# Performance work log

Measured on AMD Instinct MI355X. Metric: run time of the kernel, lower is better.

## Reference

```python
import jax, jax.numpy as jnp
import numpy as np

NUM_EMBEDDINGS = 8192
EMBEDDING_DIM = 64
N_VOXELS = 32768


def setup_inputs() -> dict:
    key = jax.random.key(0)
    k1, k2 = jax.random.split(key)
    z = jax.random.normal(k1, (N_VOXELS, EMBEDDING_DIM), dtype=jnp.float32)
    codebook = jax.random.normal(k2, (NUM_EMBEDDINGS, EMBEDDING_DIM), dtype=jnp.float32)
    return {"z": z, "codebook": codebook}


def reference(z, codebook):
    # Squared euclidean distances [N, K]; argmin is identical to argmin of cdist.
    # d2 = ||z||^2 - 2 z E^T + ||E||^2
    z_sq = jnp.sum(z * z, axis=1, keepdims=True)            # [N, 1]
    e_sq = jnp.sum(codebook * codebook, axis=1)              # [K]
    d2 = z_sq - 2.0 * (z @ codebook.T) + e_sq[None, :]       # [N, K]
    encoding_indices = jnp.argmin(d2, axis=1)                # [N] int

    quantized_feats = codebook[encoding_indices]             # [N, D] gather

    sg = jax.lax.stop_gradient
    commitment_loss = jnp.mean((z - sg(quantized_feats)) ** 2)
    vq_loss = jnp.mean((quantized_feats - sg(z)) ** 2)

    # Straight-through estimator
    quantized = z + sg(quantized_feats - z)                  # [N, D]

    return quantized, vq_loss, commitment_loss, encoding_indices
```

## Files before the change

### kernel.cpp

```cpp
#include <hip/hip_runtime.h>
#include <math.h>

#define N_VOX 32768
#define N_EMB 8192
#define DIM 64
#define NCHUNK 8
#define CODES_PER_CHUNK (N_EMB / NCHUNK)
#define TILES_PER_CHUNK (CODES_PER_CHUNK / 32)
#define NTILES (N_EMB / 32)
#define TILE_BYTES 8192
#define CHUNK_BYTES (TILES_PER_CHUNK * TILE_BYTES)

typedef _Float16 half8 __attribute__((ext_vector_type(8)));
typedef float floatx4 __attribute__((ext_vector_type(4)));

#define FP16_MIN_NORMAL 6.1035156e-5f
#define LO_SCALE 2048.0f

__global__ __launch_bounds__(256) void cbprep_kernel(const float* __restrict__ cb,
                                                     char* __restrict__ stream,
                                                     float* __restrict__ c0arr) {
    __shared__ float red[256];
    int tid  = threadIdx.x;
    int l    = tid & 63;
    int o    = tid >> 6;
    int m    = l & 31;
    int tile = blockIdx.x;
    char* tbase = stream + (size_t)tile * TILE_BYTES;
    int code = tile * 32 + m;
    int kg   = l >> 5;

    const float* p = cb + (size_t)code * DIM + o * 16 + kg * 8;
    float ss = 0.f;
    half8 h, lo;
    #pragma unroll
    for (int j = 0; j < 8; ++j) {
        float x = p[j];
        ss = fmaf(x, x, ss);
        _Float16 hi = (_Float16)x;
        float hf = (float)hi;
        if (fabsf(hf) < FP16_MIN_NORMAL) { hi = (_Float16)0.f; hf = 0.f; }
        h[j]  = hi;
        lo[j] = (_Float16)((x - hf) * LO_SCALE);
    }
    *(half8*)(tbase +        o * 1024 + l * 16) = h;
    *(half8*)(tbase + 4096 + o * 1024 + l * 16) = lo;

    red[tid] = ss;
    __syncthreads();
    if (tid < 32) {
        float s = 0.f;
        #pragma unroll
        for (int q = 0; q < 8; ++q) s += red[tid + q * 32];
        c0arr[tile * 32 + tid] = -1024.0f * s;
    }
}

__global__ __launch_bounds__(512) void scan_kernel(const float* __restrict__ z,
                                                   const char* __restrict__ stream,
                                                   const float* __restrict__ c0arr,
                                                   float* __restrict__ cand_val,
                                                   int* __restrict__ cand_idx) {
    __shared__ __align__(16) char lds[4 * TILE_BYTES + CODES_PER_CHUNK * 4];
    float* c0_lds = (float*)(lds + 4 * TILE_BYTES);
    int tid   = threadIdx.x;
    int l     = tid & 63;
    int w     = tid >> 6;
    int chunk = blockIdx.x & (NCHUNK - 1);
    int rg    = blockIdx.x >> 3;
    int lr    = l & 15;
    int lq    = l >> 4;
    int rowBase = rg * 256 + w * 32;

    half8 zh[2][2], zl[2][2], zhs[2][2];
    #pragma unroll
    for (int r = 0; r < 2; ++r) {
        #pragma unroll
        for (int h = 0; h < 2; ++h) {
            const float* p = z + (size_t)(rowBase + r * 16 + lr) * DIM + h * 32 + lq * 8;
            #pragma unroll
            for (int j = 0; j < 8; ++j) {
                float x = p[j];
                _Float16 hi = (_Float16)x;
                float hf = (float)hi;
                if (fabsf(hf) < FP16_MIN_NORMAL) { hi = (_Float16)0.f; hf = 0.f; }
                zh[r][h][j] = hi;
                zl[r][h][j] = (_Float16)((x - hf) * LO_SCALE);
            }
            zhs[r][h] = zh[r][h] * (_Float16)2048.0f;
        }
    }

    const char*  sbase = stream + (size_t)chunk * CHUNK_BYTES;
    const float* c0p   = c0arr + chunk * CODES_PER_CHUNK;

    float best[16];
    int   bt[16];
    #pragma unroll
    for (int i = 0; i < 16; ++i) { best[i] = -3.4e38f; bt[i] = 0; }

#define STAGE(gt, lb)                                                              \
    do {                                                                           \
        const char* _g = (gt) + w * 1024 + l * 16;                                 \
        char*       _d = (lb) + w * 1024 + l * 16;                                 \
        __builtin_amdgcn_global_load_lds(                                          \
            (const __attribute__((address_space(1))) void*)_g,                     \
            (__attribute__((address_space(3))) void*)_d, 16, 0, 0);                \
    } while (0)

    STAGE(sbase,                          lds);
    STAGE(sbase + (size_t)TILE_BYTES,     lds + TILE_BYTES);
    STAGE(sbase + 2 * (size_t)TILE_BYTES, lds + 2 * TILE_BYTES);
    c0_lds[tid]       = c0p[tid];
    c0_lds[tid + 512] = c0p[tid + 512];
    __syncthreads();

    for (int t = 0; t < TILES_PER_CHUNK; ++t) {
        if (t < TILES_PER_CHUNK - 2)
            asm volatile("s_waitcnt vmcnt(2)" ::: "memory");
        else if (t == TILES_PER_CHUNK - 2)
            asm volatile("s_waitcnt vmcnt(1)" ::: "memory");
        else
            asm volatile("s_waitcnt vmcnt(0)" ::: "memory");
        __builtin_amdgcn_s_barrier();
        asm volatile("" ::: "memory");

        if (t + 3 < TILES_PER_CHUNK)
            STAGE(sbase + (size_t)(t + 3) * TILE_BYTES,
                  lds + ((t + 3) & 3) * TILE_BYTES);

        const char* lb = lds + (t & 3) * TILE_BYTES;
        const char* bp = lb + 512 * lq + 16 * lr;
        half8 bh00 = *(const half8*)(bp +    0);
        half8 bh10 = *(const half8*)(bp +  256);
        half8 bh01 = *(const half8*)(bp + 2048);
        half8 bh11 = *(const half8*)(bp + 2304);
        half8 bl00 = *(const half8*)(bp + 4096);
        half8 bl10 = *(const half8*)(bp + 4352);
        half8 bl01 = *(const half8*)(bp + 6144);
        half8 bl11 = *(const half8*)(bp + 6400);
        float c00 = c0_lds[t * 32 + lr];
        float c01 = c0_lds[t * 32 + 16 + lr];

        floatx4 a00 = {c00, c00, c00, c00};
        floatx4 a01 = {c01, c01, c01, c01};
        floatx4 a10 = {c00, c00, c00, c00};
        floatx4 a11 = {c01, c01, c01, c01};

        a00 = __builtin_amdgcn_mfma_f32_16x16x32_f16(zhs[0][0], bh00, a00, 0, 0, 0);
        a01 = __builtin_amdgcn_mfma_f32_16x16x32_f16(zhs[0][0], bh10, a01, 0, 0, 0);
        a10 = __builtin_amdgcn_mfma_f32_16x16x32_f16(zhs[1][0], bh00, a10, 0, 0, 0);
        a11 = __builtin_amdgcn_mfma_f32_16x16x32_f16(zhs[1][0], bh10, a11, 0, 0, 0);
        a00 = __builtin_amdgcn_mfma_f32_16x16x32_f16(zl[0][0],  bh00, a00, 0, 0, 0);
        a01 = __builtin_amdgcn_mfma_f32_16x16x32_f16(zl[0][0],  bh10, a01, 0, 0, 0);
        a10 = __builtin_amdgcn_mfma_f32_16x16x32_f16(zl[1][0],  bh00, a10, 0, 0, 0);
        a11 = __builtin_amdgcn_mfma_f32_16x16x32_f16(zl[1][0],  bh10, a11, 0, 0, 0);
        a00 = __builtin_amdgcn_mfma_f32_16x16x32_f16(zh[0][0],  bl00, a00, 0, 0, 0);
        a01 = __builtin_amdgcn_mfma_f32_16x16x32_f16(zh[0][0],  bl10, a01, 0, 0, 0);
        a10 = __builtin_amdgcn_mfma_f32_16x16x32_f16(zh[1][0],  bl00, a10, 0, 0, 0);
        a11 = __builtin_amdgcn_mfma_f32_16x16x32_f16(zh[1][0],  bl10, a11, 0, 0, 0);
        a00 = __builtin_amdgcn_mfma_f32_16x16x32_f16(zhs[0][1], bh01, a00, 0, 0, 0);
        a01 = __builtin_amdgcn_mfma_f32_16x16x32_f16(zhs[0][1], bh11, a01, 0, 0, 0);
        a10 = __builtin_amdgcn_mfma_f32_16x16x32_f16(zhs[1][1], bh01, a10, 0, 0, 0);
        a11 = __builtin_amdgcn_mfma_f32_16x16x32_f16(zhs[1][1], bh11, a11, 0, 0, 0);
        a00 = __builtin_amdgcn_mfma_f32_16x16x32_f16(zl[0][1],  bh01, a00, 0, 0, 0);
        a01 = __builtin_amdgcn_mfma_f32_16x16x32_f16(zl[0][1],  bh11, a01, 0, 0, 0);
        a10 = __builtin_amdgcn_mfma_f32_16x16x32_f16(zl[1][1],  bh01, a10, 0, 0, 0);
        a11 = __builtin_amdgcn_mfma_f32_16x16x32_f16(zl[1][1],  bh11, a11, 0, 0, 0);
        a00 = __builtin_amdgcn_mfma_f32_16x16x32_f16(zh[0][1],  bl01, a00, 0, 0, 0);
        a01 = __builtin_amdgcn_mfma_f32_16x16x32_f16(zh[0][1],  bl11, a01, 0, 0, 0);
        a10 = __builtin_amdgcn_mfma_f32_16x16x32_f16(zh[1][1],  bl01, a10, 0, 0, 0);
        a11 = __builtin_amdgcn_mfma_f32_16x16x32_f16(zh[1][1],  bl11, a11, 0, 0, 0);

        #pragma unroll
        for (int i = 0; i < 4; ++i) {
            if (a00[i] > best[ 0 + i]) { best[ 0 + i] = a00[i]; bt[ 0 + i] = t; }
            if (a01[i] > best[ 4 + i]) { best[ 4 + i] = a01[i]; bt[ 4 + i] = t; }
            if (a10[i] > best[ 8 + i]) { best[ 8 + i] = a10[i]; bt[ 8 + i] = t; }
            if (a11[i] > best[12 + i]) { best[12 + i] = a11[i]; bt[12 + i] = t; }
        }
    }
#undef STAGE

    #pragma unroll
    for (int r = 0; r < 2; ++r) {
        #pragma unroll
        for (int i = 0; i < 4; ++i) {
            float v0 = best[r * 8 + i];     int id0 = bt[r * 8 + i] * 32 + lr;
            float v1 = best[r * 8 + 4 + i]; int id1 = bt[r * 8 + 4 + i] * 32 + 16 + lr;
            float v = v0; int id = id0;
            if (v1 > v || (v1 == v && id1 < id)) { v = v1; id = id1; }
            #pragma unroll
            for (int off = 1; off < 16; off <<= 1) {
                float ov = __shfl_xor(v, off, 64);
                int   oi = __shfl_xor(id, off, 64);
                if (ov > v || (ov == v && oi < id)) { v = ov; id = oi; }
            }
            if (lr == 0) {
                int row = rowBase + r * 16 + 4 * lq + i;
                cand_val[chunk * N_VOX + row] = v;
                cand_idx[chunk * N_VOX + row] = chunk * CODES_PER_CHUNK + id;
            }
        }
    }
}

__global__ __launch_bounds__(256) void finalize_kernel(const float* __restrict__ z,
                                                       const float* __restrict__ cb,
                                                       const float* __restrict__ cand_val,
                                                       const int* __restrict__ cand_idx,
                                                       float* __restrict__ out,
                                                       float* __restrict__ partials) {
    int g    = blockIdx.x * 256 + threadIdx.x;
    int row  = g >> 3;
    int c    = g & 7;

    float v  = cand_val[c * N_VOX + row];
    int   id = cand_idx[c * N_VOX + row];
    #pragma unroll
    for (int off = 1; off < 8; off <<= 1) {
        float ov = __shfl_xor(v, off, 8);
        int   oi = __shfl_xor(id, off, 8);
        if (ov > v || (ov == v && oi < id)) { v = ov; id = oi; }
    }

    if (c == 0)
        out[(size_t)N_VOX * DIM + 2 + row] = (float)id;

    const float4* zp = (const float4*)(z  + (size_t)row * DIM + c * 8);
    const float4* qp = (const float4*)(cb + (size_t)id  * DIM + c * 8);
    float4*       op = (float4*)(out + (size_t)row * DIM + c * 8);
    float ss = 0.f;
    #pragma unroll
    for (int d = 0; d < 2; ++d) {
        float4 zt = zp[d], qt = qp[d];
        float dx = qt.x - zt.x, dy = qt.y - zt.y;
        float dz = qt.z - zt.z, dw = qt.w - zt.w;
        float4 o;
        o.x = zt.x + dx; o.y = zt.y + dy;
        o.z = zt.z + dz; o.w = zt.w + dw;
        op[d] = o;
        ss += dx*dx + dy*dy + dz*dz + dw*dw;
    }

    __shared__ float red[256];
    red[threadIdx.x] = ss;
    __syncthreads();
    #pragma unroll
    for (int s = 128; s > 0; s >>= 1) {
        if (threadIdx.x < s) red[threadIdx.x] += red[threadIdx.x + s];
        __syncthreads();
    }
    if (threadIdx.x == 0) partials[blockIdx.x] = red[0];
}

__global__ __launch_bounds__(256) void loss_kernel(const float* __restrict__ partials,
                                                   float* __restrict__ out) {
    __shared__ float red[256];
    red[threadIdx.x] = (partials[threadIdx.x]       + partials[threadIdx.x + 256])
                     + (partials[threadIdx.x + 512] + partials[threadIdx.x + 768]);
    __syncthreads();
    #pragma unroll
    for (int st = 128; st > 0; st >>= 1) {
        if (threadIdx.x < st) red[threadIdx.x] += red[threadIdx.x + st];
        __syncthreads();
    }
    if (threadIdx.x == 0) {
        float mean = red[0] / (float)((size_t)N_VOX * DIM);
        out[(size_t)N_VOX * DIM + 0] = mean;
        out[(size_t)N_VOX * DIM + 1] = mean;
    }
}

extern "C" void kernel_launch(void* const* d_in, const int* in_sizes, int n_in,
                              void* d_out, int out_size, void* d_ws, size_t ws_size,
                              hipStream_t stream) {
    const float* z  = (const float*)d_in[0];
    const float* cb = (const float*)d_in[1];
    float* out = (float*)d_out;

    char*  bstream  = (char*)d_ws;
    float* c0arr    = (float*)(bstream + (size_t)NTILES * TILE_BYTES);
    float* cand_val = c0arr + N_EMB;
    int*   cand_idx = (int*)(cand_val + (size_t)NCHUNK * N_VOX);
    float* partials = (float*)(cand_idx + (size_t)NCHUNK * N_VOX);

    cbprep_kernel  <<<dim3(NTILES), dim3(256), 0, stream>>>(cb, bstream, c0arr);
    scan_kernel    <<<dim3((N_VOX / 256) * NCHUNK), dim3(512), 0, stream>>>(z, bstream, c0arr, cand_val, cand_idx);
    finalize_kernel<<<dim3(N_VOX * 8 / 256), dim3(256), 0, stream>>>(z, cb, cand_val, cand_idx, out, partials);
    loss_kernel    <<<1, 256, 0, stream>>>(partials, out);
}
```

Baseline: 157.7 us.

## Double-buffer LDS fragment loads in registers and raise MFMA priority

Loads the codebook fragments for the next tile from LDS into a second register set while the current tile's MFMAs run, with the loop unrolled by two so the buffers alternate. The global-to-LDS wait counts are adjusted so the next tile is resident one step earlier. MFMA sections are wrapped in s_setprio to favour matrix issue across waves. The aim is to hide LDS read latency behind the matrix instructions, at the cost of more registers and possible occupancy loss.

```diff
diff --git a/kernel.cpp b/kernel.cpp
--- a/kernel.cpp
+++ b/kernel.cpp
@@ -99,6 +99,12 @@
     #pragma unroll
     for (int i = 0; i < 16; ++i) { best[i] = -3.4e38f; bt[i] = 0; }
 
+    struct BF {
+        half8 h00, h10, h01, h11, l00, l10, l01, l11;
+        float ca, cb;
+    };
+    BF fA, fB;
+
 #define STAGE(gt, lb)                                                              \
     do {                                                                           \
         const char* _g = (gt) + w * 1024 + l * 16;                                 \
@@ -108,78 +114,95 @@
             (__attribute__((address_space(3))) void*)_d, 16, 0, 0);                \
     } while (0)
 
+#define LOADB(B, lb, tt)                                                           \
+    do {                                                                           \
+        const char* bp_ = (lb) + 512 * lq + 16 * lr;                               \
+        B.h00 = *(const half8*)(bp_ +    0);                                       \
+        B.h10 = *(const half8*)(bp_ +  256);                                       \
+        B.h01 = *(const half8*)(bp_ + 2048);                                       \
+        B.h11 = *(const half8*)(bp_ + 2304);                                       \
+        B.l00 = *(const half8*)(bp_ + 4096);                                       \
+        B.l10 = *(const half8*)(bp_ + 4352);                                       \
+        B.l01 = *(const half8*)(bp_ + 6144);                                       \
+        B.l11 = *(const half8*)(bp_ + 6400);                                       \
+        B.ca  = c0_lds[(tt) * 32 + lr];                                            \
+        B.cb  = c0_lds[(tt) * 32 + 16 + lr];                                       \
+    } while (0)
+
+#define COMPUTE(B, t)                                                              \
+    do {                                                                           \
+        floatx4 a00 = {B.ca, B.ca, B.ca, B.ca};                                    \
+        floatx4 a01 = {B.cb, B.cb, B.cb, B.cb};                                    \
+        floatx4 a10 = {B.ca, B.ca, B.ca, B.ca};                                    \
+        floatx4 a11 = {B.cb, B.cb, B.cb, B.cb};                                    \
+        __builtin_amdgcn_s_setprio(1);                                             \
+        a00 = __builtin_amdgcn_mfma_f32_16x16x32_f16(zhs[0][0], B.h00, a00, 0, 0, 0); \
+        a01 = __builtin_amdgcn_mfma_f32_16x16x32_f16(zhs[0][0], B.h10, a01, 0, 0, 0); \
+        a10 = __builtin_amdgcn_mfma_f32_16x16x32_f16(zhs[1][0], B.h00, a10, 0, 0, 0); \
+        a11 = __builtin_amdgcn_mfma_f32_16x16x32_f16(zhs[1][0], B.h10, a11, 0, 0, 0); \
+        a00 = __builtin_amdgcn_mfma_f32_16x16x32_f16(zl[0][0],  B.h00, a00, 0, 0, 0); \
+        a01 = __builtin_amdgcn_mfma_f32_16x16x32_f16(zl[0][0],  B.h10, a01, 0, 0, 0); \
+        a10 = __builtin_amdgcn_mfma_f32_16x16x32_f16(zl[1][0],  B.h00, a10, 0, 0, 0); \
+        a11 = __builtin_amdgcn_mfma_f32_16x16x32_f16(zl[1][0],  B.h10, a11, 0, 0, 0); \
+        a00 = __builtin_amdgcn_mfma_f32_16x16x32_f16(zh[0][0],  B.l00, a00, 0, 0, 0); \
+        a01 = __builtin_amdgcn_mfma_f32_16x16x32_f16(zh[0][0],  B.l10, a01, 0, 0, 0); \
+        a10 = __builtin_amdgcn_mfma_f32_16x16x32_f16(zh[1][0],  B.l00, a10, 0, 0, 0); \
+        a11 = __builtin_amdgcn_mfma_f32_16x16x32_f16(zh[1][0],  B.l10, a11, 0, 0, 0); \
+        a00 = __builtin_amdgcn_mfma_f32_16x16x32_f16(zhs[0][1], B.h01, a00, 0, 0, 0); \
+        a01 = __builtin_amdgcn_mfma_f32_16x16x32_f16(zhs[0][1], B.h11, a01, 0, 0, 0); \
+        a10 = __builtin_amdgcn_mfma_f32_16x16x32_f16(zhs[1][1], B.h01, a10, 0, 0, 0); \
+        a11 = __builtin_amdgcn_mfma_f32_16x16x32_f16(zhs[1][1], B.h11, a11, 0, 0, 0); \
+        a00 = __builtin_amdgcn_mfma_f32_16x16x32_f16(zl[0][1],  B.h01, a00, 0, 0, 0); \
+        a01 = __builtin_amdgcn_mfma_f32_16x16x32_f16(zl[0][1],  B.h11, a01, 0, 0, 0); \
+        a10 = __builtin_amdgcn_mfma_f32_16x16x32_f16(zl[1][1],  B.h01, a10, 0, 0, 0); \
+        a11 = __builtin_amdgcn_mfma_f32_16x16x32_f16(zl[1][1],  B.h11, a11, 0, 0, 0); \
+        a00 = __builtin_amdgcn_mfma_f32_16x16x32_f16(zh[0][1],  B.l01, a00, 0, 0, 0); \
+        a01 = __builtin_amdgcn_mfma_f32_16x16x32_f16(zh[0][1],  B.l11, a01, 0, 0, 0); \
+        a10 = __builtin_amdgcn_mfma_f32_16x16x32_f16(zh[1][1],  B.l01, a10, 0, 0, 0); \
+        a11 = __builtin_amdgcn_mfma_f32_16x16x32_f16(zh[1][1],  B.l11, a11, 0, 0, 0); \
+        __builtin_amdgcn_s_setprio(0);                                             \
+        _Pragma("unroll")                                                          \
+        for (int i = 0; i < 4; ++i) {                                              \
+            if (a00[i] > best[ 0 + i]) { best[ 0 + i] = a00[i]; bt[ 0 + i] = (t); } \
+            if (a01[i] > best[ 4 + i]) { best[ 4 + i] = a01[i]; bt[ 4 + i] = (t); } \
+            if (a10[i] > best[ 8 + i]) { best[ 8 + i] = a10[i]; bt[ 8 + i] = (t); } \
+            if (a11[i] > best[12 + i]) { best[12 + i] = a11[i]; bt[12 + i] = (t); } \
+        }                                                                          \
+    } while (0)
+
+#define BODY(t, CUR, NXT)                                                          \
+    do {                                                                           \
+        if ((t) < TILES_PER_CHUNK - 2)                                             \
+            asm volatile("s_waitcnt vmcnt(1)" ::: "memory");                       \
+        else                                                                       \
+            asm volatile("s_waitcnt vmcnt(0)" ::: "memory");                       \
+        __builtin_amdgcn_s_barrier();                                              \
+        asm volatile("" ::: "memory");                                             \
+        if ((t) + 3 < TILES_PER_CHUNK)                                             \
+            STAGE(sbase + (size_t)((t) + 3) * TILE_BYTES,                          \
+                  lds + (((t) + 3) & 3) * TILE_BYTES);                             \
+        if ((t) + 1 < TILES_PER_CHUNK)                                             \
+            LOADB(NXT, lds + (((t) + 1) & 3) * TILE_BYTES, (t) + 1);               \
+        COMPUTE(CUR, (t));                                                         \
+    } while (0)
+
     STAGE(sbase,                          lds);
     STAGE(sbase + (size_t)TILE_BYTES,     lds + TILE_BYTES);
     STAGE(sbase + 2 * (size_t)TILE_BYTES, lds + 2 * TILE_BYTES);
     c0_lds[tid]       = c0p[tid];
     c0_lds[tid + 512] = c0p[tid + 512];
+    asm volatile("s_waitcnt vmcnt(2)" ::: "memory");
     __syncthreads();
-
-    for (int t = 0; t < TILES_PER_CHUNK; ++t) {
-        if (t < TILES_PER_CHUNK - 2)
-            asm volatile("s_waitcnt vmcnt(2)" ::: "memory");
-        else if (t == TILES_PER_CHUNK - 2)
-            asm volatile("s_waitcnt vmcnt(1)" ::: "memory");
-        else
-            asm volatile("s_waitcnt vmcnt(0)" ::: "memory");
-        __builtin_amdgcn_s_barrier();
-        asm volatile("" ::: "memory");
-
-        if (t + 3 < TILES_PER_CHUNK)
-            STAGE(sbase + (size_t)(t + 3) * TILE_BYTES,
-                  lds + ((t + 3) & 3) * TILE_BYTES);
-
-        const char* lb = lds + (t & 3) * TILE_BYTES;
-        const char* bp = lb + 512 * lq + 16 * lr;
-        half8 bh00 = *(const half8*)(bp +    0);
-        half8 bh10 = *(const half8*)(bp +  256);
-        half8 bh01 = *(const half8*)(bp + 2048);
-        half8 bh11 = *(const half8*)(bp + 2304);
-        half8 bl00 = *(const half8*)(bp + 4096);
-        half8 bl10 = *(const half8*)(bp + 4352);
-        half8 bl01 = *(const half8*)(bp + 6144);
-        half8 bl11 = *(const half8*)(bp + 6400);
-        float c00 = c0_lds[t * 32 + lr];
-        float c01 = c0_lds[t * 32 + 16 + lr];
-
-        floatx4 a00 = {c00, c00, c00, c00};
-        floatx4 a01 = {c01, c01, c01, c01};
-        floatx4 a10 = {c00, c00, c00, c00};
-        floatx4 a11 = {c01, c01, c01, c01};
-
-        a00 = __builtin_amdgcn_mfma_f32_16x16x32_f16(zhs[0][0], bh00, a00, 0, 0, 0);
-        a01 = __builtin_amdgcn_mfma_f32_16x16x32_f16(zhs[0][0], bh10, a01, 0, 0, 0);
-        a10 = __builtin_amdgcn_mfma_f32_16x16x32_f16(zhs[1][0], bh00, a10, 0, 0, 0);
-        a11 = __builtin_amdgcn_mfma_f32_16x16x32_f16(zhs[1][0], bh10, a11, 0, 0, 0);
-        a00 = __builtin_amdgcn_mfma_f32_16x16x32_f16(zl[0][0],  bh00, a00, 0, 0, 0);
-        a01 = __builtin_amdgcn_mfma_f32_16x16x32_f16(zl[0][0],  bh10, a01, 0, 0, 0);
-        a10 = __builtin_amdgcn_mfma_f32_16x16x32_f16(zl[1][0],  bh00, a10, 0, 0, 0);
-        a11 = __builtin_amdgcn_mfma_f32_16x16x32_f16(zl[1][0],  bh10, a11, 0, 0, 0);
-        a00 = __builtin_amdgcn_mfma_f32_16x16x32_f16(zh[0][0],  bl00, a00, 0, 0, 0);
-        a01 = __builtin_amdgcn_mfma_f32_16x16x32_f16(zh[0][0],  bl10, a01, 0, 0, 0);
-        a10 = __builtin_amdgcn_mfma_f32_16x16x32_f16(zh[1][0],  bl00, a10, 0, 0, 0);
-        a11 = __builtin_amdgcn_mfma_f32_16x16x32_f16(zh[1][0],  bl10, a11, 0, 0, 0);
-        a00 = __builtin_amdgcn_mfma_f32_16x16x32_f16(zhs[0][1], bh01, a00, 0, 0, 0);
-        a01 = __builtin_amdgcn_mfma_f32_16x16x32_f16(zhs[0][1], bh11, a01, 0, 0, 0);
-        a10 = __builtin_amdgcn_mfma_f32_16x16x32_f16(zhs[1][1], bh01, a10, 0, 0, 0);
-        a11 = __builtin_amdgcn_mfma_f32_16x16x32_f16(zhs[1][1], bh11, a11, 0, 0, 0);
-        a00 = __builtin_amdgcn_mfma_f32_16x16x32_f16(zl[0][1],  bh01, a00, 0, 0, 0);
-        a01 = __builtin_amdgcn_mfma_f32_16x16x32_f16(zl[0][1],  bh11, a01, 0, 0, 0);
-        a10 = __builtin_amdgcn_mfma_f32_16x16x32_f16(zl[1][1],  bh01, a10, 0, 0, 0);
-        a11 = __builtin_amdgcn_mfma_f32_16x16x32_f16(zl[1][1],  bh11, a11, 0, 0, 0);
-        a00 = __builtin_amdgcn_mfma_f32_16x16x32_f16(zh[0][1],  bl01, a00, 0, 0, 0);
-        a01 = __builtin_amdgcn_mfma_f32_16x16x32_f16(zh[0][1],  bl11, a01, 0, 0, 0);
-        a10 = __builtin_amdgcn_mfma_f32_16x16x32_f16(zh[1][1],  bl01, a10, 0, 0, 0);
-        a11 = __builtin_amdgcn_mfma_f32_16x16x32_f16(zh[1][1],  bl11, a11, 0, 0, 0);
-
-        #pragma unroll
-        for (int i = 0; i < 4; ++i) {
-            if (a00[i] > best[ 0 + i]) { best[ 0 + i] = a00[i]; bt[ 0 + i] = t; }
-            if (a01[i] > best[ 4 + i]) { best[ 4 + i] = a01[i]; bt[ 4 + i] = t; }
-            if (a10[i] > best[ 8 + i]) { best[ 8 + i] = a10[i]; bt[ 8 + i] = t; }
-            if (a11[i] > best[12 + i]) { best[12 + i] = a11[i]; bt[12 + i] = t; }
-        }
-    }
+    LOADB(fA, lds, 0);
+
+    for (int tp = 0; tp < TILES_PER_CHUNK / 2; ++tp) {
+        int t0 = tp * 2;
+        BODY(t0,     fA, fB);
+        BODY(t0 + 1, fB, fA);
+    }
+#undef BODY
+#undef COMPUTE
+#undef LOADB
 #undef STAGE
 
     #pragma unroll
```

Result: slower. 191.0 us (+21.1%).

## Load codebook tiles directly from global memory instead of staging through LDS

Applied to the files above, without the earlier changes.

Drops the LDS ring buffer, the async global-to-LDS staging and the per-tile barriers. Each lane now reads its B fragments and bias values straight from global memory, relying on L1/L2 to serve the reuse across the 8 waves of a block. The loop is unrolled by two and the MFMA block is wrapped in s_setprio to favour matrix issue. The cost is that every wave now issues its own global loads, with exposed latency and no explicit prefetch, which could stall the MFMA pipeline.

```diff
diff --git a/kernel.cpp b/kernel.cpp
--- a/kernel.cpp
+++ b/kernel.cpp
@@ -61,8 +61,6 @@
                                                    const float* __restrict__ c0arr,
                                                    float* __restrict__ cand_val,
                                                    int* __restrict__ cand_idx) {
-    __shared__ __align__(16) char lds[4 * TILE_BYTES + CODES_PER_CHUNK * 4];
-    float* c0_lds = (float*)(lds + 4 * TILE_BYTES);
     int tid   = threadIdx.x;
     int l     = tid & 63;
     int w     = tid >> 6;
@@ -93,44 +91,16 @@
 
     const char*  sbase = stream + (size_t)chunk * CHUNK_BYTES;
     const float* c0p   = c0arr + chunk * CODES_PER_CHUNK;
+    int boff = 512 * lq + 16 * lr;
 
     float best[16];
     int   bt[16];
     #pragma unroll
     for (int i = 0; i < 16; ++i) { best[i] = -3.4e38f; bt[i] = 0; }
 
-#define STAGE(gt, lb)                                                              \
-    do {                                                                           \
-        const char* _g = (gt) + w * 1024 + l * 16;                                 \
-        char*       _d = (lb) + w * 1024 + l * 16;                                 \
-        __builtin_amdgcn_global_load_lds(                                          \
-            (const __attribute__((address_space(1))) void*)_g,                     \
-            (__attribute__((address_space(3))) void*)_d, 16, 0, 0);                \
-    } while (0)
-
-    STAGE(sbase,                          lds);
-    STAGE(sbase + (size_t)TILE_BYTES,     lds + TILE_BYTES);
-    STAGE(sbase + 2 * (size_t)TILE_BYTES, lds + 2 * TILE_BYTES);
-    c0_lds[tid]       = c0p[tid];
-    c0_lds[tid + 512] = c0p[tid + 512];
-    __syncthreads();
-
+    #pragma unroll 2
     for (int t = 0; t < TILES_PER_CHUNK; ++t) {
-        if (t < TILES_PER_CHUNK - 2)
-            asm volatile("s_waitcnt vmcnt(2)" ::: "memory");
-        else if (t == TILES_PER_CHUNK - 2)
-            asm volatile("s_waitcnt vmcnt(1)" ::: "memory");
-        else
-            asm volatile("s_waitcnt vmcnt(0)" ::: "memory");
-        __builtin_amdgcn_s_barrier();
-        asm volatile("" ::: "memory");
-
-        if (t + 3 < TILES_PER_CHUNK)
-            STAGE(sbase + (size_t)(t + 3) * TILE_BYTES,
-                  lds + ((t + 3) & 3) * TILE_BYTES);
-
-        const char* lb = lds + (t & 3) * TILE_BYTES;
-        const char* bp = lb + 512 * lq + 16 * lr;
+        const char* bp = sbase + (size_t)t * TILE_BYTES + boff;
         half8 bh00 = *(const half8*)(bp +    0);
         half8 bh10 = *(const half8*)(bp +  256);
         half8 bh01 = *(const half8*)(bp + 2048);
@@ -139,14 +109,15 @@
         half8 bl10 = *(const half8*)(bp + 4352);
         half8 bl01 = *(const half8*)(bp + 6144);
         half8 bl11 = *(const half8*)(bp + 6400);
-        float c00 = c0_lds[t * 32 + lr];
-        float c01 = c0_lds[t * 32 + 16 + lr];
+        float c00  = c0p[t * 32 + lr];
+        float c01  = c0p[t * 32 + 16 + lr];
 
         floatx4 a00 = {c00, c00, c00, c00};
         floatx4 a01 = {c01, c01, c01, c01};
         floatx4 a10 = {c00, c00, c00, c00};
         floatx4 a11 = {c01, c01, c01, c01};
 
+        __builtin_amdgcn_s_setprio(1);
         a00 = __builtin_amdgcn_mfma_f32_16x16x32_f16(zhs[0][0], bh00, a00, 0, 0, 0);
         a01 = __builtin_amdgcn_mfma_f32_16x16x32_f16(zhs[0][0], bh10, a01, 0, 0, 0);
         a10 = __builtin_amdgcn_mfma_f32_16x16x32_f16(zhs[1][0], bh00, a10, 0, 0, 0);
@@ -171,6 +142,7 @@
         a01 = __builtin_amdgcn_mfma_f32_16x16x32_f16(zh[0][1],  bl11, a01, 0, 0, 0);
         a10 = __builtin_amdgcn_mfma_f32_16x16x32_f16(zh[1][1],  bl01, a10, 0, 0, 0);
         a11 = __builtin_amdgcn_mfma_f32_16x16x32_f16(zh[1][1],  bl11, a11, 0, 0, 0);
+        __builtin_amdgcn_s_setprio(0);
 
         #pragma unroll
         for (int i = 0; i < 4; ++i) {
@@ -180,7 +152,6 @@
             if (a11[i] > best[12 + i]) { best[12 + i] = a11[i]; bt[12 + i] = t; }
         }
     }
-#undef STAGE
 
     #pragma unroll
     for (int r = 0; r < 2; ++r) {
```

Result: slower. 174.3 us (+10.5%).
